# Optimization experiments

Hardware: AMD Instinct MI355X
Metric: run time of the kernel (lower is better)

## Reference

```python
import jax, jax.numpy as jnp
import numpy as np

NEG_SLOPE = 0.2  # PyG GATConv default negative_slope


def gat_conv(x, W, b, a_src, a_dst, src, dst, N, H, C):
    """PyG-style GATConv (v1 attention), concat heads, self-loops already in (src,dst)."""
    h = (x @ W).reshape(N, H, C)                       # [N,H,C]
    al_src = jnp.sum(h * a_src, axis=-1)               # [N,H]
    al_dst = jnp.sum(h * a_dst, axis=-1)               # [N,H]
    e = jax.nn.leaky_relu(al_src[src] + al_dst[dst], NEG_SLOPE)  # [E,H]
    m = jax.ops.segment_max(e, dst, num_segments=N)    # segment softmax (stable)
    m = jnp.where(jnp.isfinite(m), m, 0.0)
    ex = jnp.exp(e - m[dst])
    denom = jax.ops.segment_sum(ex, dst, num_segments=N)
    alpha = ex / (denom[dst] + 1e-16)                  # [E,H]
    msg = h[src] * alpha[..., None]                    # [E,H,C]
    out = jax.ops.segment_sum(msg, dst, num_segments=N)  # [N,H,C]
    return out.reshape(N, H * C) + b


def setup_inputs() -> dict:
    key = jax.random.key(0)
    ks = jax.random.split(key, 16)
    N, E, IN, HID, HEADS, OUT, G = 50000, 600000, 128, 64, 4, 10, 64
    x = jax.random.normal(ks[0], (N, IN), dtype=jnp.float32)
    edge_index = jax.random.randint(ks[1], (2, E), 0, N, dtype=jnp.int32)
    batch = jnp.sort(jax.random.randint(ks[2], (N,), 0, G, dtype=jnp.int32))
    s = 0.1
    p = {
        'W1': jax.random.normal(ks[3], (IN, HEADS * HID)) * s,
        'b1': jnp.zeros((HEADS * HID,), jnp.float32),
        'asrc1': jax.random.normal(ks[4], (HEADS, HID)) * s,
        'adst1': jax.random.normal(ks[5], (HEADS, HID)) * s,
        'W2': jax.random.normal(ks[6], (HEADS * HID, HEADS * HID)) * s,
        'b2': jnp.zeros((HEADS * HID,), jnp.float32),
        'asrc2': jax.random.normal(ks[7], (HEADS, HID)) * s,
        'adst2': jax.random.normal(ks[8], (HEADS, HID)) * s,
        'W3': jax.random.normal(ks[9], (HEADS * HID, HID)) * s,
        'b3': jnp.zeros((HID,), jnp.float32),
        'asrc3': jax.random.normal(ks[10], (1, HID)) * s,
        'adst3': jax.random.normal(ks[11], (1, HID)) * s,
        'linW': jax.random.normal(ks[12], (HID, OUT)) * s,
        'linb': jnp.zeros((OUT,), jnp.float32),
    }
    return dict(x=x, edge_index=edge_index, batch=batch, **p)


def reference(x, edge_index, batch, W1, b1, asrc1, adst1, W2, b2, asrc2, adst2,
              W3, b3, asrc3, adst3, linW, linb):
    N = x.shape[0]
    G = 64  # number of graphs
    loops = jnp.arange(N, dtype=edge_index.dtype)
    src = jnp.concatenate([edge_index[0], loops])  # PyG adds self-loops by default
    dst = jnp.concatenate([edge_index[1], loops])
    # eval mode: dropout is identity
    h = jax.nn.elu(gat_conv(x, W1, b1, asrc1, adst1, src, dst, N, 4, 64))
    h = jax.nn.elu(gat_conv(h, W2, b2, asrc2, adst2, src, dst, N, 4, 64))
    h = jax.nn.elu(gat_conv(h, W3, b3, asrc3, adst3, src, dst, N, 1, 64))
    # global mean pool over graphs
    sums = jax.ops.segment_sum(h, batch, num_segments=G)            # [G,64]
    cnts = jax.ops.segment_sum(jnp.ones((N,), h.dtype), batch, num_segments=G)
    pooled = sums / jnp.maximum(cnts, 1.0)[:, None]
    return pooled @ linW + linb                                      # [G,10]
```

## Files before the change

### kernel.cpp

```cpp
#include <hip/hip_runtime.h>
#include <hip/hip_bf16.h>
#include <math.h>

#define NEG_SLOPE 0.2f

typedef short short8 __attribute__((ext_vector_type(8)));
typedef float f32x4 __attribute__((ext_vector_type(4)));
typedef unsigned int u32;
typedef unsigned short u16;

__device__ __forceinline__ float lrelu(float x){ return x > 0.f ? x : NEG_SLOPE * x; }
__device__ __forceinline__ float elu_f(float x){ return x > 0.f ? x : __expf(x) - 1.f; }
__device__ __forceinline__ float bf2f(u16 u){ return __uint_as_float(((u32)u) << 16); }
__device__ __forceinline__ u16 f2bf(float f){
  __hip_bfloat16 h = __float2bfloat16(f);
  return *(u16*)&h;
}

__global__ void prep_kernel(const float* __restrict__ x, u16* __restrict__ xb, int n4,
                            const float* __restrict__ W1, u16* __restrict__ w1t,
                            const float* __restrict__ W2, u16* __restrict__ w2t,
                            const float* __restrict__ W3, u16* __restrict__ w3t){
  int i = blockIdx.x * 256 + threadIdx.x;
  if (i < n4){
    float4 v = ((const float4*)x)[i];
    ushort4 o;
    o.x = f2bf(v.x); o.y = f2bf(v.y); o.z = f2bf(v.z); o.w = f2bf(v.w);
    ((ushort4*)xb)[i] = o;
    return;
  }
  int t = i - n4;
  if (t < 128 * 256){
    int k = t >> 8, m = t & 255;
    w1t[m * 128 + k] = f2bf(W1[t]);
    return;
  }
  t -= 128 * 256;
  if (t < 256 * 256){
    int k = t >> 8, m = t & 255;
    w2t[m * 256 + k] = f2bf(W2[t]);
    return;
  }
  t -= 256 * 256;
  if (t < 256 * 64){
    int k = t >> 6, m = t & 63;
    w3t[m * 256 + k] = f2bf(W3[t]);
  }
}

__global__ void hist_kernel(const int* __restrict__ dst, int E, int N, int* counts){
  int i = blockIdx.x * 256 + threadIdx.x;
  if (i < E + N){
    int d = (i < E) ? dst[i] : (i - E);
    atomicAdd(&counts[d], 1);
  }
}

__global__ void scan_block_kernel(const int* __restrict__ counts, int* __restrict__ rp,
                                  int* __restrict__ bsums, int N){
  __shared__ int s[256];
  int i = blockIdx.x * 256 + threadIdx.x;
  int v = (i < N) ? counts[i] : 0;
  s[threadIdx.x] = v;
  __syncthreads();
  for (int off = 1; off < 256; off <<= 1){
    int t = (threadIdx.x >= off) ? s[threadIdx.x - off] : 0;
    __syncthreads();
    s[threadIdx.x] += t;
    __syncthreads();
  }
  if (i < N) rp[i] = s[threadIdx.x] - v;
  if (threadIdx.x == 255) bsums[blockIdx.x] = s[255];
}

__global__ void scan_sums_kernel(int* bsums, int nb, int* total){
  __shared__ int s[256];
  int v = (threadIdx.x < nb) ? bsums[threadIdx.x] : 0;
  s[threadIdx.x] = v;
  __syncthreads();
  for (int off = 1; off < 256; off <<= 1){
    int t = (threadIdx.x >= off) ? s[threadIdx.x - off] : 0;
    __syncthreads();
    s[threadIdx.x] += t;
    __syncthreads();
  }
  if (threadIdx.x < nb) bsums[threadIdx.x] = s[threadIdx.x] - v;
  if (threadIdx.x == 255) *total = s[255];
}

__global__ void scan_add_kernel(int* __restrict__ rp, int* __restrict__ cur,
                                const int* __restrict__ bsums,
                                const int* __restrict__ total, int N){
  int i = blockIdx.x * 256 + threadIdx.x;
  if (i < N){
    int v = rp[i] + bsums[blockIdx.x];
    rp[i] = v;
    cur[i] = v;
  }
  if (i == 0) rp[N] = *total;
}

__global__ void scatter_kernel(const int* __restrict__ src, const int* __restrict__ dst,
                               int E, int N, int* cursor, int* __restrict__ edge_src){
  int i = blockIdx.x * 256 + threadIdx.x;
  if (i < E + N){
    int s, d;
    if (i < E){ s = src[i]; d = dst[i]; }
    else      { s = i - E;  d = i - E;  }
    int pos = atomicAdd(&cursor[d], 1);
    edge_src[pos] = s;
  }
}

template<int BN>
__global__ __launch_bounds__(256) void gemm_mfma(const u16* __restrict__ A,
                                                 const u16* __restrict__ Bt,
                                                 u16* __restrict__ C,
                                                 const float* __restrict__ asrc,
                                                 const float* __restrict__ adst,
                                                 float* __restrict__ als,
                                                 float* __restrict__ ald,
                                                 int N, int K, int M){
  constexpr int BM = 128;
  constexpr int MI = (BN == 128) ? 4 : 2;
  constexpr int SB = BN * 8 / 256;
  constexpr int HH = (BN == 128) ? 4 : 1;
  __shared__ short As[8][BM][8];
  __shared__ short Bs[8][BN][8];
  const int tid = threadIdx.x;
  const int w = tid >> 6, lane = tid & 63;
  const int quad = lane >> 4, l16 = lane & 15;
  const int row0 = blockIdx.y * BM, col0 = blockIdx.x * BN;
  const int wrow = (BN == 128) ? (w >> 1) * 64 : w * 32;
  const int wcol = (BN == 128) ? (w & 1) * 64 : 0;

  f32x4 acc[MI][4];
#pragma unroll
  for (int i = 0; i < MI; i++)
#pragma unroll
    for (int j = 0; j < 4; j++) acc[i][j] = (f32x4){0.f, 0.f, 0.f, 0.f};

  for (int k0 = 0; k0 < K; k0 += 64){
    __syncthreads();
#pragma unroll
    for (int q = 0; q < 4; q++){
      int lb = q * 256 + w * 64;
      int li = lb + lane;
      int c = li >> 7, r = li & 127;
      int grow = min(row0 + r, N - 1);
      const u16* gp = A + (size_t)grow * K + k0 + c * 8;
      __builtin_amdgcn_global_load_lds((const __attribute__((address_space(1))) void*)gp,
                                       (__attribute__((address_space(3))) void*)((char*)&As[0][0][0] + (size_t)lb * 16),
                                       16, 0, 0);
    }
#pragma unroll
    for (int q = 0; q < SB; q++){
      int lb = q * 256 + w * 64;
      int li = lb + lane;
      int c = li / BN, n = li % BN;
      const u16* gp = Bt + (size_t)(col0 + n) * K + k0 + c * 8;
      __builtin_amdgcn_global_load_lds((const __attribute__((address_space(1))) void*)gp,
                                       (__attribute__((address_space(3))) void*)((char*)&Bs[0][0][0] + (size_t)lb * 16),
                                       16, 0, 0);
    }
    __syncthreads();
#pragma unroll
    for (int ks = 0; ks < 2; ks++){
      short8 a[MI], b[4];
#pragma unroll
      for (int i = 0; i < MI; i++) a[i] = *(const short8*)&As[ks * 4 + quad][wrow + i * 16 + l16][0];
#pragma unroll
      for (int j = 0; j < 4; j++)  b[j] = *(const short8*)&Bs[ks * 4 + quad][wcol + j * 16 + l16][0];
#pragma unroll
      for (int i = 0; i < MI; i++)
#pragma unroll
        for (int j = 0; j < 4; j++)
          acc[i][j] = __builtin_amdgcn_mfma_f32_16x16x32_bf16(a[i], b[j], acc[i][j], 0, 0, 0);
    }
  }

  const int head = (col0 + wcol) >> 6;
  float avs[4], avd[4];
#pragma unroll
  for (int j = 0; j < 4; j++){
    int c = j * 16 + l16;
    avs[j] = asrc[head * 64 + c];
    avd[j] = adst[head * 64 + c];
  }

#pragma unroll
  for (int i = 0; i < MI; i++){
#pragma unroll
    for (int rr = 0; rr < 4; rr++){
      int row = row0 + wrow + i * 16 + quad * 4 + rr;
      float ps = acc[i][0][rr] * avs[0] + acc[i][1][rr] * avs[1]
               + acc[i][2][rr] * avs[2] + acc[i][3][rr] * avs[3];
      float pd = acc[i][0][rr] * avd[0] + acc[i][1][rr] * avd[1]
               + acc[i][2][rr] * avd[2] + acc[i][3][rr] * avd[3];
#pragma unroll
      for (int off = 8; off > 0; off >>= 1){
        ps += __shfl_xor(ps, off);
        pd += __shfl_xor(pd, off);
      }
      if (row < N){
#pragma unroll
        for (int j = 0; j < 4; j++)
          C[(size_t)row * M + col0 + wcol + j * 16 + l16] = f2bf(acc[i][j][rr]);
        if (l16 == 0){
          als[(size_t)row * HH + head] = ps;
          ald[(size_t)row * HH + head] = pd;
        }
      }
    }
  }
}

template<bool OBF>
__global__ __launch_bounds__(256) void agg4_kernel(const u16* __restrict__ hb,
    const float* __restrict__ als, const float* __restrict__ ald,
    const int* __restrict__ row_ptr, const int* __restrict__ edge_src,
    const float* __restrict__ bias, void* __restrict__ outv, int N){
  __shared__ float lex[4][256];
  __shared__ int lu[4][64];
  int wslot = threadIdx.x >> 6;
  int node = (blockIdx.x * 256 + threadIdx.x) >> 6;
  int lane = threadIdx.x & 63;
  if (node >= N) return;
  int beg = row_ptr[node], end = row_ptr[node + 1];
  int deg = end - beg;
  float4 t4 = *(const float4*)(ald + node * 4);

  float m0 = -1e30f, m1 = -1e30f, m2 = -1e30f, m3 = -1e30f;
  int u_mine = 0;
  float e0 = -1e30f, e1 = -1e30f, e2 = -1e30f, e3 = -1e30f;
  for (int c0 = 0; c0 < deg; c0 += 64){
    int j = c0 + lane;
    bool v = j < deg;
    int u = v ? edge_src[beg + j] : 0;
    float4 s = v ? *(const float4*)(als + (size_t)u * 4)
                 : make_float4(-1e30f, -1e30f, -1e30f, -1e30f);
    float f0 = lrelu(s.x + t4.x), f1 = lrelu(s.y + t4.y);
    float f2 = lrelu(s.z + t4.z), f3 = lrelu(s.w + t4.w);
    m0 = fmaxf(m0, f0); m1 = fmaxf(m1, f1);
    m2 = fmaxf(m2, f2); m3 = fmaxf(m3, f3);
    if (c0 == 0){ u_mine = u; e0 = f0; e1 = f1; e2 = f2; e3 = f3; }
  }
#pragma unroll
  for (int off = 32; off > 0; off >>= 1){
    m0 = fmaxf(m0, __shfl_xor(m0, off)); m1 = fmaxf(m1, __shfl_xor(m1, off));
    m2 = fmaxf(m2, __shfl_xor(m2, off)); m3 = fmaxf(m3, __shfl_xor(m3, off));
  }
  const int hh = lane >> 4;
  float a0 = 0.f, a1 = 0.f, a2 = 0.f, a3 = 0.f, denom = 0.f;
  const u16* hbl = hb + lane * 4;

  for (int c0 = 0; c0 < deg; c0 += 64){
    int cnt = min(64, deg - c0);
    int u; float f0, f1, f2, f3;
    if (c0 == 0){ u = u_mine; f0 = e0; f1 = e1; f2 = e2; f3 = e3; }
    else {
      int j = c0 + lane;
      bool v = j < deg;
      u = v ? edge_src[beg + j] : 0;
      float4 s = v ? *(const float4*)(als + (size_t)u * 4)
                   : make_float4(-1e30f, -1e30f, -1e30f, -1e30f);
      f0 = lrelu(s.x + t4.x); f1 = lrelu(s.y + t4.y);
      f2 = lrelu(s.z + t4.z); f3 = lrelu(s.w + t4.w);
    }
    float4 exv;
    exv.x = __expf(f0 - m0); exv.y = __expf(f1 - m1);
    exv.z = __expf(f2 - m2); exv.w = __expf(f3 - m3);
    *(float4*)&lex[wslot][lane * 4] = exv;
    lu[wslot][lane] = u;
    asm volatile("s_waitcnt lgkmcnt(0)" ::: "memory");
#pragma unroll 4
    for (int j = 0; j < cnt; j++){
      float ex = lex[wslot][j * 4 + hh];
      int uu = lu[wslot][j];
      uint2 t = *(const uint2*)(hbl + (size_t)uu * 256);
      denom += ex;
      a0 += ex * __uint_as_float((t.x & 0xffffu) << 16);
      a1 += ex * __uint_as_float(t.x & 0xffff0000u);
      a2 += ex * __uint_as_float((t.y & 0xffffu) << 16);
      a3 += ex * __uint_as_float(t.y & 0xffff0000u);
    }
    asm volatile("" ::: "memory");
  }
  float inv = 1.f / (denom + 1e-16f);
  int ch = lane * 4;
  float o0 = elu_f(a0 * inv + bias[ch]);
  float o1 = elu_f(a1 * inv + bias[ch + 1]);
  float o2 = elu_f(a2 * inv + bias[ch + 2]);
  float o3 = elu_f(a3 * inv + bias[ch + 3]);
  if (OBF){
    uint2 o;
    o.x = (u32)f2bf(o0) | ((u32)f2bf(o1) << 16);
    o.y = (u32)f2bf(o2) | ((u32)f2bf(o3) << 16);
    ((uint2*)outv)[(size_t)node * 64 + lane] = o;
  } else {
    *(float4*)((float*)outv + (size_t)node * 256 + ch) = make_float4(o0, o1, o2, o3);
  }
}

__global__ __launch_bounds__(256) void agg1_kernel(const u16* __restrict__ hb,
    const float* __restrict__ als, const float* __restrict__ ald,
    const int* __restrict__ row_ptr, const int* __restrict__ edge_src,
    const float* __restrict__ bias, float* __restrict__ out, int N){
  __shared__ float lex[4][64];
  __shared__ int lu[4][64];
  int wslot = threadIdx.x >> 6;
  int node = (blockIdx.x * 256 + threadIdx.x) >> 6;
  int lane = threadIdx.x & 63;
  if (node >= N) return;
  int beg = row_ptr[node], end = row_ptr[node + 1];
  int deg = end - beg;
  float adv = ald[node];
  float m = -1e30f;
  int u_mine = 0; float e_mine = -1e30f;
  for (int c0 = 0; c0 < deg; c0 += 64){
    int j = c0 + lane;
    bool v = j < deg;
    int u = v ? edge_src[beg + j] : 0;
    float e = v ? lrelu(als[u] + adv) : -1e30f;
    m = fmaxf(m, e);
    if (c0 == 0){ u_mine = u; e_mine = e; }
  }
#pragma unroll
  for (int off = 32; off > 0; off >>= 1) m = fmaxf(m, __shfl_xor(m, off));
  int eo = lane >> 4;
  int chb = (lane & 15) * 4;
  float a0 = 0.f, a1 = 0.f, a2 = 0.f, a3 = 0.f, denom = 0.f;
  for (int c0 = 0; c0 < deg; c0 += 64){
    int cnt = min(64, deg - c0);
    int u; float e;
    if (c0 == 0){ u = u_mine; e = e_mine; }
    else {
      int j = c0 + lane;
      bool v = j < deg;
      u = v ? edge_src[beg + j] : 0;
      e = v ? lrelu(als[u] + adv) : -1e30f;
    }
    lex[wslot][lane] = __expf(e - m);
    lu[wslot][lane] = u;
    asm volatile("s_waitcnt lgkmcnt(0)" ::: "memory");
#pragma unroll 4
    for (int j = 0; j < cnt; j += 4){
      int jj = j + eo;
      bool valid = jj < cnt;
      float ex = valid ? lex[wslot][jj] : 0.f;
      int uu = lu[wslot][jj];
      uint2 t = *(const uint2*)(hb + (size_t)uu * 64 + chb);
      denom += ex;
      a0 += ex * __uint_as_float((t.x & 0xffffu) << 16);
      a1 += ex * __uint_as_float(t.x & 0xffff0000u);
      a2 += ex * __uint_as_float((t.y & 0xffffu) << 16);
      a3 += ex * __uint_as_float(t.y & 0xffff0000u);
    }
    asm volatile("" ::: "memory");
  }
#pragma unroll
  for (int off = 16; off < 64; off <<= 1){
    denom += __shfl_xor(denom, off);
    a0 += __shfl_xor(a0, off); a1 += __shfl_xor(a1, off);
    a2 += __shfl_xor(a2, off); a3 += __shfl_xor(a3, off);
  }
  if (eo == 0){
    float inv = 1.f / (denom + 1e-16f);
    float o0 = elu_f(a0 * inv + bias[chb]);
    float o1 = elu_f(a1 * inv + bias[chb + 1]);
    float o2 = elu_f(a2 * inv + bias[chb + 2]);
    float o3 = elu_f(a3 * inv + bias[chb + 3]);
    *(float4*)(out + (size_t)node * 64 + chb) = make_float4(o0, o1, o2, o3);
  }
}

__global__ void pool_kernel(const float* __restrict__ f, const int* __restrict__ batch,
                            float* sums, int* cnts, int N){
  int lane = threadIdx.x;
  int s = blockIdx.x * 128;
  if (s >= N) return;
  int e = min(s + 128, N);
  float acc = 0.f;
  int cnt = 0;
  int cur = batch[s];
  for (int n = s; n < e; n++){
    int g = batch[n];
    if (g != cur){
      atomicAdd(&sums[cur * 64 + lane], acc);
      if (lane == 0) atomicAdd(&cnts[cur], cnt);
      acc = 0.f; cnt = 0; cur = g;
    }
    acc += f[(size_t)n * 64 + lane];
    cnt++;
  }
  atomicAdd(&sums[cur * 64 + lane], acc);
  if (lane == 0) atomicAdd(&cnts[cur], cnt);
}

__global__ void final_kernel(const float* __restrict__ sums, const int* __restrict__ cnts,
                             const float* __restrict__ linW, const float* __restrict__ linb,
                             float* __restrict__ out){
  int t = threadIdx.x;
  if (t >= 640) return;
  int g = t / 10, o = t % 10;
  float c = fmaxf((float)cnts[g], 1.f);
  float acc = 0.f;
#pragma unroll
  for (int k = 0; k < 64; k++) acc += sums[g * 64 + k] * linW[k * 10 + o];
  out[t] = acc / c + linb[o];
}

extern "C" void kernel_launch(void* const* d_in, const int* in_sizes, int n_in,
                              void* d_out, int out_size, void* d_ws, size_t ws_size,
                              hipStream_t stream) {
  const float* x     = (const float*)d_in[0];
  const int*   ei    = (const int*)  d_in[1];
  const int*   batch = (const int*)  d_in[2];
  const float* W1    = (const float*)d_in[3];
  const float* b1    = (const float*)d_in[4];
  const float* asrc1 = (const float*)d_in[5];
  const float* adst1 = (const float*)d_in[6];
  const float* W2    = (const float*)d_in[7];
  const float* b2    = (const float*)d_in[8];
  const float* asrc2 = (const float*)d_in[9];
  const float* adst2 = (const float*)d_in[10];
  const float* W3    = (const float*)d_in[11];
  const float* b3    = (const float*)d_in[12];
  const float* asrc3 = (const float*)d_in[13];
  const float* adst3 = (const float*)d_in[14];
  const float* linW  = (const float*)d_in[15];
  const float* linb  = (const float*)d_in[16];

  const int N = in_sizes[0] / 128;
  const int E = in_sizes[1] / 2;
  const int Etot = E + N;
  const int G = 64;
  const int* src = ei;
  const int* dst = ei + E;

  char* p = (char*)d_ws;
  auto carve = [&](size_t bytes) -> char* {
    char* r = p;
    p += (bytes + 255) & ~(size_t)255;
    return r;
  };
  u16*   xb       = (u16*)  carve((size_t)N * 128 * 2);
  u16*   w1t      = (u16*)  carve((size_t)256 * 128 * 2);
  u16*   w2t      = (u16*)  carve((size_t)256 * 256 * 2);
  u16*   w3t      = (u16*)  carve((size_t)64 * 256 * 2);
  u16*   hb       = (u16*)  carve((size_t)N * 256 * 2);
  u16*   featb    = (u16*)  carve((size_t)N * 256 * 2);
  float* out3     = (float*)carve((size_t)N * 64 * 4);
  float* als      = (float*)carve((size_t)N * 4 * 4);
  float* ald      = (float*)carve((size_t)N * 4 * 4);
  int*   counts   = (int*)  carve((size_t)N * 4);
  int*   row_ptr  = (int*)  carve((size_t)(N + 1) * 4);
  int*   cursor   = (int*)  carve((size_t)N * 4);
  int*   edge_src = (int*)  carve((size_t)Etot * 4);
  int*   bsums    = (int*)  carve(256 * 4);
  int*   total    = (int*)  carve(256);
  float* sums     = (float*)carve((size_t)G * 64 * 4);
  int*   cnts     = (int*)  carve((size_t)G * 4);

  const int nb = (N + 255) / 256;
  const int n4 = N * 128 / 4;
  const int prep_items = n4 + 128 * 256 + 256 * 256 + 256 * 64;

  prep_kernel<<<(prep_items + 255) / 256, 256, 0, stream>>>(x, xb, n4, W1, w1t, W2, w2t, W3, w3t);

  hipMemsetAsync(counts, 0, (size_t)N * 4, stream);
  hist_kernel<<<(Etot + 255) / 256, 256, 0, stream>>>(dst, E, N, counts);
  scan_block_kernel<<<nb, 256, 0, stream>>>(counts, row_ptr, bsums, N);
  scan_sums_kernel<<<1, 256, 0, stream>>>(bsums, nb, total);
  scan_add_kernel<<<nb, 256, 0, stream>>>(row_ptr, cursor, bsums, total, N);
  scatter_kernel<<<(Etot + 255) / 256, 256, 0, stream>>>(src, dst, E, N, cursor, edge_src);

  const int nby = (N + 127) / 128;
  const int wpn_grid = (N + 3) / 4;

  gemm_mfma<128><<<dim3(2, nby), 256, 0, stream>>>(xb, w1t, hb, asrc1, adst1, als, ald, N, 128, 256);
  agg4_kernel<true><<<wpn_grid, 256, 0, stream>>>(hb, als, ald, row_ptr, edge_src, b1, featb, N);

  gemm_mfma<128><<<dim3(2, nby), 256, 0, stream>>>(featb, w2t, hb, asrc2, adst2, als, ald, N, 256, 256);
  agg4_kernel<true><<<wpn_grid, 256, 0, stream>>>(hb, als, ald, row_ptr, edge_src, b2, featb, N);

  gemm_mfma<64><<<dim3(1, nby), 256, 0, stream>>>(featb, w3t, hb, asrc3, adst3, als, ald, N, 256, 64);
  agg1_kernel<<<wpn_grid, 256, 0, stream>>>(hb, als, ald, row_ptr, edge_src, b3, out3, N);

  hipMemsetAsync(sums, 0, (size_t)G * 64 * 4, stream);
  hipMemsetAsync(cnts, 0, (size_t)G * 4, stream);
  pool_kernel<<<(N + 127) / 128, 64, 0, stream>>>(out3, batch, sums, cnts, N);
  final_kernel<<<1, 640, 0, stream>>>(sums, cnts, linW, linb, (float*)d_out);
}
```

Before: 416.3 us.

## Drop softmax max pass, fuse pooling into agg1, merge scan and memset launches

The aggregation kernels no longer run a separate pass to compute the per-node max logit. They exponentiate the leaky-relu scores directly, which saves a second gather of edge sources and source scores per node. Mean pooling is folded into the last aggregation kernel through per-node float atomics into the graph sums, which removes the out3 buffer and the pool kernel. The two scan-finish kernels become one, and the memsets are folded into the prep kernel. The trade-off is overflow risk in the unnormalised exp for large logits, heavy atomic contention on the 64 graph accumulators, and a pooled sum that is no longer deterministic.

Result: slower. 689.3 us (+65.6%).

```diff
diff --git a/kernel.cpp b/kernel.cpp
--- a/kernel.cpp
+++ b/kernel.cpp
@@ -20,7 +20,9 @@
 __global__ void prep_kernel(const float* __restrict__ x, u16* __restrict__ xb, int n4,
                             const float* __restrict__ W1, u16* __restrict__ w1t,
                             const float* __restrict__ W2, u16* __restrict__ w2t,
-                            const float* __restrict__ W3, u16* __restrict__ w3t){
+                            const float* __restrict__ W3, u16* __restrict__ w3t,
+                            int* __restrict__ counts, int N,
+                            float* __restrict__ sums, int* __restrict__ cnts){
   int i = blockIdx.x * 256 + threadIdx.x;
   if (i < n4){
     float4 v = ((const float4*)x)[i];
@@ -45,7 +47,14 @@
   if (t < 256 * 64){
     int k = t >> 6, m = t & 63;
     w3t[m * 256 + k] = f2bf(W3[t]);
-  }
+    return;
+  }
+  t -= 256 * 64;
+  if (t < N){ counts[t] = 0; return; }
+  t -= N;
+  if (t < 64 * 64){ sums[t] = 0.f; return; }
+  t -= 64 * 64;
+  if (t < 64) cnts[t] = 0;
 }
 
 __global__ void hist_kernel(const int* __restrict__ dst, int E, int N, int* counts){
@@ -73,31 +82,28 @@
   if (threadIdx.x == 255) bsums[blockIdx.x] = s[255];
 }
 
-__global__ void scan_sums_kernel(int* bsums, int nb, int* total){
-  __shared__ int s[256];
-  int v = (threadIdx.x < nb) ? bsums[threadIdx.x] : 0;
-  s[threadIdx.x] = v;
+__global__ void scan_finish_kernel(int* __restrict__ rp, int* __restrict__ cur,
+                                   const int* __restrict__ bsums, int nb, int N){
+  __shared__ int red[8];
+  int b = blockIdx.x, t = threadIdx.x;
+  int w = t >> 6, lane = t & 63;
+  int v = (t < nb) ? bsums[t] : 0;
+  int pre = (t < b) ? v : 0;
+#pragma unroll
+  for (int off = 32; off > 0; off >>= 1){
+    pre += __shfl_xor(pre, off);
+    v   += __shfl_xor(v, off);
+  }
+  if (lane == 0){ red[w] = pre; red[4 + w] = v; }
   __syncthreads();
-  for (int off = 1; off < 256; off <<= 1){
-    int t = (threadIdx.x >= off) ? s[threadIdx.x - off] : 0;
-    __syncthreads();
-    s[threadIdx.x] += t;
-    __syncthreads();
-  }
-  if (threadIdx.x < nb) bsums[threadIdx.x] = s[threadIdx.x] - v;
-  if (threadIdx.x == 255) *total = s[255];
-}
-
-__global__ void scan_add_kernel(int* __restrict__ rp, int* __restrict__ cur,
-                                const int* __restrict__ bsums,
-                                const int* __restrict__ total, int N){
-  int i = blockIdx.x * 256 + threadIdx.x;
+  int offset = red[0] + red[1] + red[2] + red[3];
+  int i = b * 256 + t;
   if (i < N){
-    int v = rp[i] + bsums[blockIdx.x];
-    rp[i] = v;
-    cur[i] = v;
-  }
-  if (i == 0) rp[N] = *total;
+    int val = rp[i] + offset;
+    rp[i] = val;
+    cur[i] = val;
+  }
+  if (b == 0 && t == 0) rp[N] = red[4] + red[5] + red[6] + red[7];
 }
 
 __global__ void scatter_kernel(const int* __restrict__ src, const int* __restrict__ dst,
@@ -226,57 +232,30 @@
   int node = (blockIdx.x * 256 + threadIdx.x) >> 6;
   int lane = threadIdx.x & 63;
   if (node >= N) return;
-  int beg = row_ptr[node], end = row_ptr[node + 1];
-  int deg = end - beg;
+  int beg = row_ptr[node];
+  int deg = row_ptr[node + 1] - beg;
   float4 t4 = *(const float4*)(ald + node * 4);
-
-  float m0 = -1e30f, m1 = -1e30f, m2 = -1e30f, m3 = -1e30f;
-  int u_mine = 0;
-  float e0 = -1e30f, e1 = -1e30f, e2 = -1e30f, e3 = -1e30f;
-  for (int c0 = 0; c0 < deg; c0 += 64){
-    int j = c0 + lane;
-    bool v = j < deg;
-    int u = v ? edge_src[beg + j] : 0;
-    float4 s = v ? *(const float4*)(als + (size_t)u * 4)
-                 : make_float4(-1e30f, -1e30f, -1e30f, -1e30f);
-    float f0 = lrelu(s.x + t4.x), f1 = lrelu(s.y + t4.y);
-    float f2 = lrelu(s.z + t4.z), f3 = lrelu(s.w + t4.w);
-    m0 = fmaxf(m0, f0); m1 = fmaxf(m1, f1);
-    m2 = fmaxf(m2, f2); m3 = fmaxf(m3, f3);
-    if (c0 == 0){ u_mine = u; e0 = f0; e1 = f1; e2 = f2; e3 = f3; }
-  }
-#pragma unroll
-  for (int off = 32; off > 0; off >>= 1){
-    m0 = fmaxf(m0, __shfl_xor(m0, off)); m1 = fmaxf(m1, __shfl_xor(m1, off));
-    m2 = fmaxf(m2, __shfl_xor(m2, off)); m3 = fmaxf(m3, __shfl_xor(m3, off));
-  }
   const int hh = lane >> 4;
   float a0 = 0.f, a1 = 0.f, a2 = 0.f, a3 = 0.f, denom = 0.f;
   const u16* hbl = hb + lane * 4;
 
   for (int c0 = 0; c0 < deg; c0 += 64){
     int cnt = min(64, deg - c0);
-    int u; float f0, f1, f2, f3;
-    if (c0 == 0){ u = u_mine; f0 = e0; f1 = e1; f2 = e2; f3 = e3; }
-    else {
-      int j = c0 + lane;
-      bool v = j < deg;
-      u = v ? edge_src[beg + j] : 0;
-      float4 s = v ? *(const float4*)(als + (size_t)u * 4)
-                   : make_float4(-1e30f, -1e30f, -1e30f, -1e30f);
-      f0 = lrelu(s.x + t4.x); f1 = lrelu(s.y + t4.y);
-      f2 = lrelu(s.z + t4.z); f3 = lrelu(s.w + t4.w);
-    }
+    int j = c0 + lane;
+    int u = (j < deg) ? edge_src[beg + j] : 0;
+    float4 s = *(const float4*)(als + (size_t)u * 4);
     float4 exv;
-    exv.x = __expf(f0 - m0); exv.y = __expf(f1 - m1);
-    exv.z = __expf(f2 - m2); exv.w = __expf(f3 - m3);
+    exv.x = __expf(lrelu(s.x + t4.x));
+    exv.y = __expf(lrelu(s.y + t4.y));
+    exv.z = __expf(lrelu(s.z + t4.z));
+    exv.w = __expf(lrelu(s.w + t4.w));
     *(float4*)&lex[wslot][lane * 4] = exv;
     lu[wslot][lane] = u;
     asm volatile("s_waitcnt lgkmcnt(0)" ::: "memory");
-#pragma unroll 4
-    for (int j = 0; j < cnt; j++){
-      float ex = lex[wslot][j * 4 + hh];
-      int uu = lu[wslot][j];
+#pragma unroll 8
+    for (int jj = 0; jj < cnt; jj++){
+      float ex = lex[wslot][jj * 4 + hh];
+      int uu = lu[wslot][jj];
       uint2 t = *(const uint2*)(hbl + (size_t)uu * 256);
       denom += ex;
       a0 += ex * __uint_as_float((t.x & 0xffffu) << 16);
@@ -305,49 +284,32 @@
 __global__ __launch_bounds__(256) void agg1_kernel(const u16* __restrict__ hb,
     const float* __restrict__ als, const float* __restrict__ ald,
     const int* __restrict__ row_ptr, const int* __restrict__ edge_src,
-    const float* __restrict__ bias, float* __restrict__ out, int N){
+    const float* __restrict__ bias, const int* __restrict__ batch,
+    float* __restrict__ sums, int* __restrict__ cnts, int N){
   __shared__ float lex[4][64];
   __shared__ int lu[4][64];
   int wslot = threadIdx.x >> 6;
   int node = (blockIdx.x * 256 + threadIdx.x) >> 6;
   int lane = threadIdx.x & 63;
   if (node >= N) return;
-  int beg = row_ptr[node], end = row_ptr[node + 1];
-  int deg = end - beg;
+  int beg = row_ptr[node];
+  int deg = row_ptr[node + 1] - beg;
   float adv = ald[node];
-  float m = -1e30f;
-  int u_mine = 0; float e_mine = -1e30f;
-  for (int c0 = 0; c0 < deg; c0 += 64){
-    int j = c0 + lane;
-    bool v = j < deg;
-    int u = v ? edge_src[beg + j] : 0;
-    float e = v ? lrelu(als[u] + adv) : -1e30f;
-    m = fmaxf(m, e);
-    if (c0 == 0){ u_mine = u; e_mine = e; }
-  }
-#pragma unroll
-  for (int off = 32; off > 0; off >>= 1) m = fmaxf(m, __shfl_xor(m, off));
   int eo = lane >> 4;
   int chb = (lane & 15) * 4;
   float a0 = 0.f, a1 = 0.f, a2 = 0.f, a3 = 0.f, denom = 0.f;
   for (int c0 = 0; c0 < deg; c0 += 64){
     int cnt = min(64, deg - c0);
-    int u; float e;
-    if (c0 == 0){ u = u_mine; e = e_mine; }
-    else {
-      int j = c0 + lane;
-      bool v = j < deg;
-      u = v ? edge_src[beg + j] : 0;
-      e = v ? lrelu(als[u] + adv) : -1e30f;
-    }
-    lex[wslot][lane] = __expf(e - m);
+    int j = c0 + lane;
+    bool v = j < deg;
+    int u = v ? edge_src[beg + j] : 0;
+    lex[wslot][lane] = v ? __expf(lrelu(als[u] + adv)) : 0.f;
     lu[wslot][lane] = u;
     asm volatile("s_waitcnt lgkmcnt(0)" ::: "memory");
 #pragma unroll 4
-    for (int j = 0; j < cnt; j += 4){
-      int jj = j + eo;
-      bool valid = jj < cnt;
-      float ex = valid ? lex[wslot][jj] : 0.f;
+    for (int j2 = 0; j2 < cnt; j2 += 4){
+      int jj = j2 + eo;
+      float ex = lex[wslot][jj];
       int uu = lu[wslot][jj];
       uint2 t = *(const uint2*)(hb + (size_t)uu * 64 + chb);
       denom += ex;
@@ -370,31 +332,14 @@
     float o1 = elu_f(a1 * inv + bias[chb + 1]);
     float o2 = elu_f(a2 * inv + bias[chb + 2]);
     float o3 = elu_f(a3 * inv + bias[chb + 3]);
-    *(float4*)(out + (size_t)node * 64 + chb) = make_float4(o0, o1, o2, o3);
-  }
-}
-
-__global__ void pool_kernel(const float* __restrict__ f, const int* __restrict__ batch,
-                            float* sums, int* cnts, int N){
-  int lane = threadIdx.x;
-  int s = blockIdx.x * 128;
-  if (s >= N) return;
-  int e = min(s + 128, N);
-  float acc = 0.f;
-  int cnt = 0;
-  int cur = batch[s];
-  for (int n = s; n < e; n++){
-    int g = batch[n];
-    if (g != cur){
-      atomicAdd(&sums[cur * 64 + lane], acc);
-      if (lane == 0) atomicAdd(&cnts[cur], cnt);
-      acc = 0.f; cnt = 0; cur = g;
-    }
-    acc += f[(size_t)n * 64 + lane];
-    cnt++;
-  }
-  atomicAdd(&sums[cur * 64 + lane], acc);
-  if (lane == 0) atomicAdd(&cnts[cur], cnt);
+    int g = batch[node];
+    float* sp = sums + (size_t)g * 64 + chb;
+    atomicAdd(sp,     o0);
+    atomicAdd(sp + 1, o1);
+    atomicAdd(sp + 2, o2);
+    atomicAdd(sp + 3, o3);
+    if (lane == 0) atomicAdd(&cnts[g], 1);
+  }
 }
 
 __global__ void final_kernel(const float* __restrict__ sums, const int* __restrict__ cnts,
@@ -450,7 +395,6 @@
   u16*   w3t      = (u16*)  carve((size_t)64 * 256 * 2);
   u16*   hb       = (u16*)  carve((size_t)N * 256 * 2);
   u16*   featb    = (u16*)  carve((size_t)N * 256 * 2);
-  float* out3     = (float*)carve((size_t)N * 64 * 4);
   float* als      = (float*)carve((size_t)N * 4 * 4);
   float* ald      = (float*)carve((size_t)N * 4 * 4);
   int*   counts   = (int*)  carve((size_t)N * 4);
@@ -458,21 +402,19 @@
   int*   cursor   = (int*)  carve((size_t)N * 4);
   int*   edge_src = (int*)  carve((size_t)Etot * 4);
   int*   bsums    = (int*)  carve(256 * 4);
-  int*   total    = (int*)  carve(256);
   float* sums     = (float*)carve((size_t)G * 64 * 4);
   int*   cnts     = (int*)  carve((size_t)G * 4);
 
   const int nb = (N + 255) / 256;
   const int n4 = N * 128 / 4;
-  const int prep_items = n4 + 128 * 256 + 256 * 256 + 256 * 64;
-
-  prep_kernel<<<(prep_items + 255) / 256, 256, 0, stream>>>(x, xb, n4, W1, w1t, W2, w2t, W3, w3t);
-
-  hipMemsetAsync(counts, 0, (size_t)N * 4, stream);
+  const int prep_items = n4 + 128 * 256 + 256 * 256 + 256 * 64 + N + G * 64 + G;
+
+  prep_kernel<<<(prep_items + 255) / 256, 256, 0, stream>>>(x, xb, n4, W1, w1t, W2, w2t, W3, w3t,
+                                                            counts, N, sums, cnts);
+
   hist_kernel<<<(Etot + 255) / 256, 256, 0, stream>>>(dst, E, N, counts);
   scan_block_kernel<<<nb, 256, 0, stream>>>(counts, row_ptr, bsums, N);
-  scan_sums_kernel<<<1, 256, 0, stream>>>(bsums, nb, total);
-  scan_add_kernel<<<nb, 256, 0, stream>>>(row_ptr, cursor, bsums, total, N);
+  scan_finish_kernel<<<nb, 256, 0, stream>>>(row_ptr, cursor, bsums, nb, N);
   scatter_kernel<<<(Etot + 255) / 256, 256, 0, stream>>>(src, dst, E, N, cursor, edge_src);
 
   const int nby = (N + 127) / 128;
@@ -485,10 +427,7 @@
   agg4_kernel<true><<<wpn_grid, 256, 0, stream>>>(hb, als, ald, row_ptr, edge_src, b2, featb, N);
 
   gemm_mfma<64><<<dim3(1, nby), 256, 0, stream>>>(featb, w3t, hb, asrc3, adst3, als, ald, N, 256, 64);
-  agg1_kernel<<<wpn_grid, 256, 0, stream>>>(hb, als, ald, row_ptr, edge_src, b3, out3, N);
-
-  hipMemsetAsync(sums, 0, (size_t)G * 64 * 4, stream);
-  hipMemsetAsync(cnts, 0, (size_t)G * 4, stream);
-  pool_kernel<<<(N + 127) / 128, 64, 0, stream>>>(out3, batch, sums, cnts, N);
+  agg1_kernel<<<wpn_grid, 256, 0, stream>>>(hb, als, ald, row_ptr, edge_src, b3, batch, sums, cnts, N);
+
   final_kernel<<<1, 640, 0, stream>>>(sums, cnts, linW, linb, (float*)d_out);
 }
```
